# Performance work log

Measured on AMD Instinct MI355X. Metric: run time of the kernel, lower is better.

The kernel has to match this reference:

```python
import jax, jax.numpy as jnp
import numpy as np

CH_IN, CH_Y = 32, 16
B, H, W = 16, 256, 256


def setup_inputs() -> dict:
    key = jax.random.key(0)
    ks = jax.random.split(key, 10)
    scale_in = 1.0 / np.sqrt(CH_IN)
    scale_y = 1.0 / np.sqrt(CH_Y)
    return {
        "c": jax.random.normal(ks[0], (B, CH_IN, H, W), dtype=jnp.float32),
        "p": jax.random.normal(ks[1], (B, CH_IN, H, W), dtype=jnp.float32),
        "Wq": jax.random.uniform(ks[2], (CH_Y, CH_IN), jnp.float32, -scale_in, scale_in),
        "bq": jax.random.uniform(ks[3], (CH_Y,), jnp.float32, -scale_in, scale_in),
        "Wk": jax.random.uniform(ks[4], (CH_Y, CH_IN), jnp.float32, -scale_in, scale_in),
        "bk": jax.random.uniform(ks[5], (CH_Y,), jnp.float32, -scale_in, scale_in),
        "Wv": jax.random.uniform(ks[6], (CH_Y, CH_IN), jnp.float32, -scale_in, scale_in),
        "bv": jax.random.uniform(ks[7], (CH_Y,), jnp.float32, -scale_in, scale_in),
        "Wy": jax.random.uniform(ks[8], (CH_IN, CH_Y), jnp.float32, -scale_y, scale_y),
        "by": jax.random.uniform(ks[9], (CH_IN,), jnp.float32, -scale_y, scale_y),
    }


def _conv1x1(x, w, b):
    # x: [B,C,H,W], w: [O,C], b: [O] -> [B,O,H,W]
    return jnp.einsum("bchw,oc->bohw", x, w) + b[None, :, None, None]


def reference(c, p, Wq, bq, Wk, bk, Wv, bv, Wy, by):
    q = _conv1x1(c, Wq, bq)
    k = _conv1x1(p, Wk, bk)
    v = _conv1x1(p, Wv, bv)
    y = jax.nn.softmax(q * k, axis=-1)  # softmax over width
    y = y * v
    y = _conv1x1(y, Wy, by)
    return jnp.concatenate((y, c), axis=1)  # [B, 2*CH_IN, H, W]
```

## Files before the change

### kernel.cpp

```cpp
#include <hip/hip_runtime.h>

#define CH_IN 32
#define CH_Y  16
#define Bn    16
#define Hn    256
#define Wn    256
#define HW    (Hn * Wn)

template<int ctrl, int rm, int bm>
__device__ __forceinline__ float dpp0(float x) {
    union { float f; int i; } u, r;
    u.f = x;
    r.i = __builtin_amdgcn_update_dpp(0, u.i, ctrl, rm, bm, false);
    return r.f;
}

__device__ __forceinline__ float wave_sum64(float x) {
    x += dpp0<0x111, 0xf, 0xf>(x);
    x += dpp0<0x112, 0xf, 0xf>(x);
    x += dpp0<0x114, 0xf, 0xf>(x);
    x += dpp0<0x118, 0xf, 0xf>(x);
    x += dpp0<0x142, 0xa, 0xf>(x);
    x += dpp0<0x143, 0xc, 0xf>(x);
    union { float f; int i; } u, r;
    u.f = x;
    r.i = __builtin_amdgcn_readlane(u.i, 63);
    return r.f;
}

__global__ __launch_bounds__(256)
void CrossModalAttn_kernel(
    const float* __restrict__ cin, const float* __restrict__ pin,
    const float* __restrict__ Wq,  const float* __restrict__ bq,
    const float* __restrict__ Wk,  const float* __restrict__ bk,
    const float* __restrict__ Wv,  const float* __restrict__ bv,
    const float* __restrict__ Wy,  const float* __restrict__ by,
    float* __restrict__ out)
{
    const int bh   = blockIdx.x;
    const int b    = bh >> 8;
    const int h    = bh & 255;
    const int w    = threadIdx.x;
    const int lane = threadIdx.x & 63;
    const int wave = threadIdx.x >> 6;

    const size_t rowoff = (size_t)h * Wn + w;
    const float* pbase = pin + (size_t)b * CH_IN * HW + rowoff;
    const float* cbase = cin + (size_t)b * CH_IN * HW + rowoff;
    float*       obase = out + (size_t)b * (2 * CH_IN) * HW + rowoff;

    float pv[CH_IN];
    #pragma unroll
    for (int cc = 0; cc < CH_IN; ++cc)
        pv[cc] = pbase[(size_t)cc * HW];

    float kk[CH_Y], vv[CH_Y];
    #pragma unroll
    for (int o = 0; o < CH_Y; ++o) {
        float ka = bk[o];
        float va = bv[o];
        #pragma unroll
        for (int cc = 0; cc < CH_IN; ++cc) {
            ka = fmaf(Wk[o * CH_IN + cc], pv[cc], ka);
            va = fmaf(Wv[o * CH_IN + cc], pv[cc], va);
        }
        kk[o] = ka;
        vv[o] = va;
    }

    float qq[CH_Y];
    #pragma unroll
    for (int o = 0; o < CH_Y; ++o) qq[o] = bq[o];

    #pragma unroll
    for (int cc = 0; cc < CH_IN; ++cc) {
        float x = cbase[(size_t)cc * HW];
        obase[(size_t)(CH_IN + cc) * HW] = x;
        #pragma unroll
        for (int o = 0; o < CH_Y; ++o)
            qq[o] = fmaf(Wq[o * CH_IN + cc], x, qq[o]);
    }

    float ee[CH_Y];
    float wsum[CH_Y];
    #pragma unroll
    for (int o = 0; o < CH_Y; ++o) {
        float e = __expf(qq[o] * kk[o]);
        ee[o] = e;
        wsum[o] = wave_sum64(e);
    }

    __shared__ float4 redsum4[CH_Y];
    if (lane == 0) {
        #pragma unroll
        for (int o = 0; o < CH_Y; ++o)
            ((float*)&redsum4[o])[wave] = wsum[o];
    }
    __syncthreads();

    float yat[CH_Y];
    #pragma unroll
    for (int o = 0; o < CH_Y; ++o) {
        float4 r = redsum4[o];
        float tot = (r.x + r.y) + (r.z + r.w);
        yat[o] = ee[o] * __builtin_amdgcn_rcpf(tot) * vv[o];
    }

    #pragma unroll
    for (int cc = 0; cc < CH_IN; ++cc) {
        float acc = by[cc];
        #pragma unroll
        for (int o = 0; o < CH_Y; ++o)
            acc = fmaf(Wy[cc * CH_Y + o], yat[o], acc);
        obase[(size_t)cc * HW] = acc;
    }
}

extern "C" void kernel_launch(void* const* d_in, const int* in_sizes, int n_in,
                              void* d_out, int out_size, void* d_ws, size_t ws_size,
                              hipStream_t stream) {
    const float* c  = (const float*)d_in[0];
    const float* p  = (const float*)d_in[1];
    const float* Wq = (const float*)d_in[2];
    const float* bq = (const float*)d_in[3];
    const float* Wk = (const float*)d_in[4];
    const float* bk = (const float*)d_in[5];
    const float* Wv = (const float*)d_in[6];
    const float* bv = (const float*)d_in[7];
    const float* Wy = (const float*)d_in[8];
    const float* by = (const float*)d_in[9];
    float* out = (float*)d_out;

    dim3 grid(Bn * Hn);
    dim3 block(Wn);
    hipLaunchKernelGGL(CrossModalAttn_kernel, grid, block, 0, stream,
                       c, p, Wq, bq, Wk, bk, Wv, bv, Wy, by, out);
}
```

Before: 525.9 us.

## Use one wave per row with float4 pixels per lane and drop LDS reduction

Each block becomes a single 64-lane wave handling a full image row, with every lane processing four adjacent pixels through 128-bit vector loads and stores. The softmax denominator then comes from a single wave-level DPP reduction, which removes the shared-memory exchange and the block barrier. The p input is read twice, once for K and once for V, to keep register pressure down, and nontemporal loads and stores are used for the streaming c copy and the output. The risks are higher register use per lane and the second p read, which relies on it hitting in cache.

```diff
diff --git a/kernel.cpp b/kernel.cpp
--- a/kernel.cpp
+++ b/kernel.cpp
@@ -6,6 +6,8 @@
 #define Hn    256
 #define Wn    256
 #define HW    (Hn * Wn)
+
+typedef float f32x4 __attribute__((ext_vector_type(4)));
 
 template<int ctrl, int rm, int bm>
 __device__ __forceinline__ float dpp0(float x) {
@@ -28,7 +30,7 @@
     return r.f;
 }
 
-__global__ __launch_bounds__(256)
+__global__ __launch_bounds__(64, 3)
 void CrossModalAttn_kernel(
     const float* __restrict__ cin, const float* __restrict__ pin,
     const float* __restrict__ Wq,  const float* __restrict__ bq,
@@ -40,79 +42,111 @@
     const int bh   = blockIdx.x;
     const int b    = bh >> 8;
     const int h    = bh & 255;
-    const int w    = threadIdx.x;
-    const int lane = threadIdx.x & 63;
-    const int wave = threadIdx.x >> 6;
+    const int lane = threadIdx.x;
+    const int w0   = lane << 2;
 
-    const size_t rowoff = (size_t)h * Wn + w;
+    const size_t rowoff = (size_t)h * Wn + w0;
     const float* pbase = pin + (size_t)b * CH_IN * HW + rowoff;
     const float* cbase = cin + (size_t)b * CH_IN * HW + rowoff;
     float*       obase = out + (size_t)b * (2 * CH_IN) * HW + rowoff;
 
-    float pv[CH_IN];
-    #pragma unroll
-    for (int cc = 0; cc < CH_IN; ++cc)
-        pv[cc] = pbase[(size_t)cc * HW];
-
-    float kk[CH_Y], vv[CH_Y];
+    f32x4 qq[CH_Y];
     #pragma unroll
     for (int o = 0; o < CH_Y; ++o) {
-        float ka = bk[o];
-        float va = bv[o];
+        float t = bq[o];
+        qq[o] = (f32x4){t, t, t, t};
+    }
+    #pragma unroll 4
+    for (int cc = 0; cc < CH_IN; ++cc) {
+        f32x4 x = __builtin_nontemporal_load(
+            (const f32x4*)(cbase + (size_t)cc * HW));
+        __builtin_nontemporal_store(
+            x, (f32x4*)(obase + (size_t)(CH_IN + cc) * HW));
         #pragma unroll
-        for (int cc = 0; cc < CH_IN; ++cc) {
-            ka = fmaf(Wk[o * CH_IN + cc], pv[cc], ka);
-            va = fmaf(Wv[o * CH_IN + cc], pv[cc], va);
+        for (int o = 0; o < CH_Y; ++o) {
+            float wgt = Wq[o * CH_IN + cc];
+            qq[o].x = fmaf(wgt, x.x, qq[o].x);
+            qq[o].y = fmaf(wgt, x.y, qq[o].y);
+            qq[o].z = fmaf(wgt, x.z, qq[o].z);
+            qq[o].w = fmaf(wgt, x.w, qq[o].w);
         }
-        kk[o] = ka;
-        vv[o] = va;
     }
 
-    float qq[CH_Y];
+    f32x4 kk[CH_Y];
     #pragma unroll
-    for (int o = 0; o < CH_Y; ++o) qq[o] = bq[o];
-
-    #pragma unroll
+    for (int o = 0; o < CH_Y; ++o) {
+        float t = bk[o];
+        kk[o] = (f32x4){t, t, t, t};
+    }
+    #pragma unroll 4
     for (int cc = 0; cc < CH_IN; ++cc) {
-        float x = cbase[(size_t)cc * HW];
-        obase[(size_t)(CH_IN + cc) * HW] = x;
+        f32x4 x = *(const f32x4*)(pbase + (size_t)cc * HW);
         #pragma unroll
-        for (int o = 0; o < CH_Y; ++o)
-            qq[o] = fmaf(Wq[o * CH_IN + cc], x, qq[o]);
+        for (int o = 0; o < CH_Y; ++o) {
+            float wgt = Wk[o * CH_IN + cc];
+            kk[o].x = fmaf(wgt, x.x, kk[o].x);
+            kk[o].y = fmaf(wgt, x.y, kk[o].y);
+            kk[o].z = fmaf(wgt, x.z, kk[o].z);
+            kk[o].w = fmaf(wgt, x.w, kk[o].w);
+        }
     }
 
-    float ee[CH_Y];
-    float wsum[CH_Y];
+    f32x4 ee[CH_Y];
     #pragma unroll
     for (int o = 0; o < CH_Y; ++o) {
-        float e = __expf(qq[o] * kk[o]);
+        f32x4 e;
+        e.x = __expf(qq[o].x * kk[o].x);
+        e.y = __expf(qq[o].y * kk[o].y);
+        e.z = __expf(qq[o].z * kk[o].z);
+        e.w = __expf(qq[o].w * kk[o].w);
+        float s   = (e.x + e.y) + (e.z + e.w);
+        float tot = wave_sum64(s);
+        float r   = __builtin_amdgcn_rcpf(tot);
+        e.x *= r; e.y *= r; e.z *= r; e.w *= r;
         ee[o] = e;
-        wsum[o] = wave_sum64(e);
     }
 
-    __shared__ float4 redsum4[CH_Y];
-    if (lane == 0) {
-        #pragma unroll
-        for (int o = 0; o < CH_Y; ++o)
-            ((float*)&redsum4[o])[wave] = wsum[o];
-    }
-    __syncthreads();
-
-    float yat[CH_Y];
+    f32x4 vv[CH_Y];
     #pragma unroll
     for (int o = 0; o < CH_Y; ++o) {
-        float4 r = redsum4[o];
-        float tot = (r.x + r.y) + (r.z + r.w);
-        yat[o] = ee[o] * __builtin_amdgcn_rcpf(tot) * vv[o];
+        float t = bv[o];
+        vv[o] = (f32x4){t, t, t, t};
+    }
+    #pragma unroll 4
+    for (int cc = 0; cc < CH_IN; ++cc) {
+        f32x4 x = *(const f32x4*)(pbase + (size_t)cc * HW);
+        #pragma unroll
+        for (int o = 0; o < CH_Y; ++o) {
+            float wgt = Wv[o * CH_IN + cc];
+            vv[o].x = fmaf(wgt, x.x, vv[o].x);
+            vv[o].y = fmaf(wgt, x.y, vv[o].y);
+            vv[o].z = fmaf(wgt, x.z, vv[o].z);
+            vv[o].w = fmaf(wgt, x.w, vv[o].w);
+        }
     }
 
     #pragma unroll
-    for (int cc = 0; cc < CH_IN; ++cc) {
-        float acc = by[cc];
+    for (int o = 0; o < CH_Y; ++o) {
+        ee[o].x *= vv[o].x;
+        ee[o].y *= vv[o].y;
+        ee[o].z *= vv[o].z;
+        ee[o].w *= vv[o].w;
+    }
+
+    #pragma unroll 4
+    for (int co = 0; co < CH_IN; ++co) {
+        float t = by[co];
+        f32x4 acc = (f32x4){t, t, t, t};
         #pragma unroll
-        for (int o = 0; o < CH_Y; ++o)
-            acc = fmaf(Wy[cc * CH_Y + o], yat[o], acc);
-        obase[(size_t)cc * HW] = acc;
+        for (int o = 0; o < CH_Y; ++o) {
+            float wgt = Wy[co * CH_Y + o];
+            acc.x = fmaf(wgt, ee[o].x, acc.x);
+            acc.y = fmaf(wgt, ee[o].y, acc.y);
+            acc.z = fmaf(wgt, ee[o].z, acc.z);
+            acc.w = fmaf(wgt, ee[o].w, acc.w);
+        }
+        __builtin_nontemporal_store(
+            acc, (f32x4*)(obase + (size_t)co * HW));
     }
 }
 
@@ -132,7 +166,7 @@
     float* out = (float*)d_out;
 
     dim3 grid(Bn * Hn);
-    dim3 block(Wn);
+    dim3 block(64);
     hipLaunchKernelGGL(CrossModalAttn_kernel, grid, block, 0, stream,
                        c, p, Wq, bq, Wk, bk, Wv, bv, Wy, by, out);
 }
```

New measurement: 477.6 us. 1.1x faster.

## Process two pixels per thread with float2 loads and nontemporal stores

Applied to the files above, without the earlier changes.

Each thread now handles two adjacent width positions, with 128 threads per row block, using 8-byte vector loads and nontemporal stores. Each scalar weight load is reused across two pixels. The cross-wave reduction drops to two partial sums, and the partially unrolled channel loops reorder the q, k and v computation. This is meant to cut instruction overhead and weight-load traffic in a memory-bound kernel, at the cost of more registers per thread and fewer waves per block.

```diff
diff --git a/kernel.cpp b/kernel.cpp
--- a/kernel.cpp
+++ b/kernel.cpp
@@ -6,6 +6,8 @@
 #define Hn    256
 #define Wn    256
 #define HW    (Hn * Wn)
+
+typedef float f32x2 __attribute__((ext_vector_type(2)));
 
 template<int ctrl, int rm, int bm>
 __device__ __forceinline__ float dpp0(float x) {
@@ -28,7 +30,7 @@
     return r.f;
 }
 
-__global__ __launch_bounds__(256)
+__global__ __launch_bounds__(128, 4)
 void CrossModalAttn_kernel(
     const float* __restrict__ cin, const float* __restrict__ pin,
     const float* __restrict__ Wq,  const float* __restrict__ bq,
@@ -40,79 +42,89 @@
     const int bh   = blockIdx.x;
     const int b    = bh >> 8;
     const int h    = bh & 255;
-    const int w    = threadIdx.x;
-    const int lane = threadIdx.x & 63;
-    const int wave = threadIdx.x >> 6;
+    const int t    = threadIdx.x;
+    const int wave = t >> 6;
+    const int lane = t & 63;
+    const int w0   = t << 1;
 
-    const size_t rowoff = (size_t)h * Wn + w;
+    const size_t rowoff = (size_t)h * Wn + w0;
     const float* pbase = pin + (size_t)b * CH_IN * HW + rowoff;
     const float* cbase = cin + (size_t)b * CH_IN * HW + rowoff;
     float*       obase = out + (size_t)b * (2 * CH_IN) * HW + rowoff;
 
-    float pv[CH_IN];
-    #pragma unroll
-    for (int cc = 0; cc < CH_IN; ++cc)
-        pv[cc] = pbase[(size_t)cc * HW];
+    __shared__ float red[2 * CH_Y];
 
-    float kk[CH_Y], vv[CH_Y];
+    f32x2 qe[CH_Y];
     #pragma unroll
     for (int o = 0; o < CH_Y; ++o) {
-        float ka = bk[o];
-        float va = bv[o];
+        float ti = bq[o];
+        qe[o] = (f32x2){ti, ti};
+    }
+    #pragma unroll 8
+    for (int cc = 0; cc < CH_IN; ++cc) {
+        f32x2 x = *(const f32x2*)(cbase + (size_t)cc * HW);
+        __builtin_nontemporal_store(
+            x, (f32x2*)(obase + (size_t)(CH_IN + cc) * HW));
         #pragma unroll
-        for (int cc = 0; cc < CH_IN; ++cc) {
-            ka = fmaf(Wk[o * CH_IN + cc], pv[cc], ka);
-            va = fmaf(Wv[o * CH_IN + cc], pv[cc], va);
+        for (int o = 0; o < CH_Y; ++o) {
+            float wgt = Wq[o * CH_IN + cc];
+            qe[o].x = fmaf(wgt, x.x, qe[o].x);
+            qe[o].y = fmaf(wgt, x.y, qe[o].y);
         }
-        kk[o] = ka;
-        vv[o] = va;
     }
 
-    float qq[CH_Y];
+    f32x2 kk[CH_Y], vv[CH_Y];
     #pragma unroll
-    for (int o = 0; o < CH_Y; ++o) qq[o] = bq[o];
+    for (int o = 0; o < CH_Y; ++o) {
+        float tk = bk[o], tv = bv[o];
+        kk[o] = (f32x2){tk, tk};
+        vv[o] = (f32x2){tv, tv};
+    }
+    #pragma unroll 8
+    for (int cc = 0; cc < CH_IN; ++cc) {
+        f32x2 x = *(const f32x2*)(pbase + (size_t)cc * HW);
+        #pragma unroll
+        for (int o = 0; o < CH_Y; ++o) {
+            float wk = Wk[o * CH_IN + cc];
+            float wv = Wv[o * CH_IN + cc];
+            kk[o].x = fmaf(wk, x.x, kk[o].x);
+            kk[o].y = fmaf(wk, x.y, kk[o].y);
+            vv[o].x = fmaf(wv, x.x, vv[o].x);
+            vv[o].y = fmaf(wv, x.y, vv[o].y);
+        }
+    }
 
     #pragma unroll
-    for (int cc = 0; cc < CH_IN; ++cc) {
-        float x = cbase[(size_t)cc * HW];
-        obase[(size_t)(CH_IN + cc) * HW] = x;
-        #pragma unroll
-        for (int o = 0; o < CH_Y; ++o)
-            qq[o] = fmaf(Wq[o * CH_IN + cc], x, qq[o]);
-    }
-
-    float ee[CH_Y];
-    float wsum[CH_Y];
-    #pragma unroll
     for (int o = 0; o < CH_Y; ++o) {
-        float e = __expf(qq[o] * kk[o]);
-        ee[o] = e;
-        wsum[o] = wave_sum64(e);
-    }
-
-    __shared__ float4 redsum4[CH_Y];
-    if (lane == 0) {
-        #pragma unroll
-        for (int o = 0; o < CH_Y; ++o)
-            ((float*)&redsum4[o])[wave] = wsum[o];
+        f32x2 e;
+        e.x = __expf(qe[o].x * kk[o].x);
+        e.y = __expf(qe[o].y * kk[o].y);
+        float ws = wave_sum64(e.x + e.y);
+        if (lane == 0) red[wave * CH_Y + o] = ws;
+        qe[o] = e;
     }
     __syncthreads();
 
-    float yat[CH_Y];
     #pragma unroll
     for (int o = 0; o < CH_Y; ++o) {
-        float4 r = redsum4[o];
-        float tot = (r.x + r.y) + (r.z + r.w);
-        yat[o] = ee[o] * __builtin_amdgcn_rcpf(tot) * vv[o];
+        float tot = red[o] + red[CH_Y + o];
+        float r = __builtin_amdgcn_rcpf(tot);
+        qe[o].x *= r * vv[o].x;
+        qe[o].y *= r * vv[o].y;
     }
 
-    #pragma unroll
-    for (int cc = 0; cc < CH_IN; ++cc) {
-        float acc = by[cc];
+    #pragma unroll 8
+    for (int co = 0; co < CH_IN; ++co) {
+        float ti = by[co];
+        f32x2 acc = (f32x2){ti, ti};
         #pragma unroll
-        for (int o = 0; o < CH_Y; ++o)
-            acc = fmaf(Wy[cc * CH_Y + o], yat[o], acc);
-        obase[(size_t)cc * HW] = acc;
+        for (int o = 0; o < CH_Y; ++o) {
+            float wgt = Wy[co * CH_Y + o];
+            acc.x = fmaf(wgt, qe[o].x, acc.x);
+            acc.y = fmaf(wgt, qe[o].y, acc.y);
+        }
+        __builtin_nontemporal_store(
+            acc, (f32x2*)(obase + (size_t)co * HW));
     }
 }
 
@@ -132,7 +144,7 @@
     float* out = (float*)d_out;
 
     dim3 grid(Bn * Hn);
-    dim3 block(Wn);
+    dim3 block(128);
     hipLaunchKernelGGL(CrossModalAttn_kernel, grid, block, 0, stream,
                        c, p, Wq, bq, Wk, bk, Wv, bv, Wy, by, out);
 }
```

Measured after the change: 469.6 us. -10.7%, faster.
